# Kernel tuning notes

Hardware: AMD Instinct MI355X
Metric: run time of the kernel (lower is better)

## Reference

```python
import jax, jax.numpy as jnp
import numpy as np

N_OBJ, N_REL = 5000, 20000
HID, POOL, N_RELCLS, N_OBJCLS = 512, 4096, 51, 151


def setup_inputs() -> dict:
    key = jax.random.key(0)
    ks = jax.random.split(key, 8)
    s = lambda fi, fo: (2.0 / (fi + fo)) ** 0.5  # xavier-ish scale
    return {
        'edge_ctx': jax.random.normal(ks[0], (N_OBJ, HID), jnp.float32),
        'union_features': jax.random.normal(ks[1], (N_REL, POOL), jnp.float32),
        'W_pe': jax.random.normal(ks[2], (2 * HID, HID), jnp.float32) * (10.0 * (1.0 / HID) ** 0.5),
        'b_pe': jnp.zeros((2 * HID,), jnp.float32),
        'W_pc': jax.random.normal(ks[3], (POOL, 2 * HID), jnp.float32) * s(2 * HID, POOL),
        'b_pc': jnp.zeros((POOL,), jnp.float32),
        'W_cc': jax.random.normal(ks[4], (N_RELCLS, POOL), jnp.float32) * s(POOL, N_RELCLS),
        'b_cc': jnp.zeros((N_RELCLS,), jnp.float32),
        'freq_emb': jax.random.normal(ks[5], (N_OBJCLS * N_OBJCLS, N_RELCLS), jnp.float32) * 0.1,
        'obj_preds': jax.random.randint(ks[6], (N_OBJ,), 0, N_OBJCLS, jnp.int64 if jax.config.jax_enable_x64 else jnp.int32),
        'pair_idx': jax.random.randint(ks[7], (N_REL, 2), 0, N_OBJ, jnp.int64 if jax.config.jax_enable_x64 else jnp.int32),
    }


def reference(edge_ctx, union_features, W_pe, b_pe, W_pc, b_pc, W_cc, b_cc,
              freq_emb, obj_preds, pair_idx):
    # post_emb -> relu -> split into head/tail halves ([N,2,HID] view)
    edge_rep = jax.nn.relu(edge_ctx @ W_pe.T + b_pe)          # [N, 2*HID]
    head_rep, tail_rep = edge_rep[:, :HID], edge_rep[:, HID:]

    hi, ti = pair_idx[:, 0], pair_idx[:, 1]
    prod = jnp.concatenate([head_rep[hi], tail_rep[ti]], axis=-1)  # [R, 2*HID]
    prod_rep = prod @ W_pc.T + b_pc                               # [R, POOL]

    ctx_dists = (prod_rep * union_features) @ W_cc.T + b_cc      # [R, 51]

    # frequency bias: embedding lookup at head_cls * num_obj_cls + tail_cls
    pair_lbl = obj_preds[hi] * N_OBJCLS + obj_preds[ti]
    frq_dists = freq_emb[pair_lbl]                               # [R, 51]
    # dropout p=0.3 is identity in eval mode
    return ctx_dists + frq_dists
```

## Files before the change

### kernel.cpp

```cpp
#include <hip/hip_runtime.h>

typedef unsigned short u16;
typedef unsigned int u32;
typedef __attribute__((ext_vector_type(4))) float f32x4;
typedef __attribute__((ext_vector_type(8))) __bf16 bf16x8;
typedef __attribute__((ext_vector_type(8))) u16 u16x8;

__device__ __forceinline__ u16 f2bf(float x) {
  u32 u = __float_as_uint(x);
  u32 r = (u + 0x7FFFu + ((u >> 16) & 1u)) >> 16;
  return (u16)r;
}

__device__ __forceinline__ float bf2f(u16 b) {
  return __uint_as_float((u32)b << 16);
}

__device__ __forceinline__ void gl16(const void* g, void* l) {
  auto* gp = (__attribute__((address_space(1))) u32*)(g);
  auto* lp = (__attribute__((address_space(3))) u32*)(l);
  __builtin_amdgcn_global_load_lds(gp, lp, 16, 0, 0);
}

__device__ __forceinline__ f32x4 mfma16(bf16x8 a, bf16x8 b, f32x4 c) {
  return __builtin_amdgcn_mfma_f32_16x16x32_bf16(a, b, c, 0, 0, 0);
}

__device__ __forceinline__ u16x8 cvt8(const float* p) {
  float4 a = *(const float4*)p, b = *(const float4*)(p + 4);
  u16x8 v;
  v[0] = f2bf(a.x); v[1] = f2bf(a.y); v[2] = f2bf(a.z); v[3] = f2bf(a.w);
  v[4] = f2bf(b.x); v[5] = f2bf(b.y); v[6] = f2bf(b.z); v[7] = f2bf(b.w);
  return v;
}

__global__ void k_prep(const float* __restrict__ ec, const float* __restrict__ wpe,
                       const float* __restrict__ wpc, const float* __restrict__ wcc,
                       u16* __restrict__ ecb, u16* __restrict__ wpeb,
                       u16* __restrict__ wpcb, u16* __restrict__ wccb) {
  int i = blockIdx.x * 256 + threadIdx.x;
  if (i < 320000) {
    *(u16x8*)(ecb + (long)i * 8) = cvt8(ec + (long)i * 8);
  } else if (i < 385536) {
    int j = i - 320000;
    *(u16x8*)(wpeb + (long)j * 8) = cvt8(wpe + (long)j * 8);
  } else if (i < 909824) {
    int j = i - 385536;
    *(u16x8*)(wpcb + (long)j * 8) = cvt8(wpc + (long)j * 8);
  } else if (i < 942592) {
    int j = i - 909824;
    long base = (long)j * 8;
    int row = (int)(base >> 12);
    int col = (int)(base & 4095);
    u16x8 v;
    if (row < 51) {
      v = cvt8(wcc + (long)row * 4096 + col);
    } else {
#pragma unroll
      for (int k = 0; k < 8; ++k) v[k] = 0;
    }
    *(u16x8*)(wccb + base) = v;
  }
}

__device__ __forceinline__ void cstep(const char* sA, const char* sB,
                                      const int (&aOff)[4], const int (&bOff)[4],
                                      f32x4 (&acc)[4][4]) {
  bf16x8 af[4], bv[4];
#pragma unroll
  for (int mi = 0; mi < 4; ++mi) af[mi] = *(const bf16x8*)(sA + aOff[mi]);
#pragma unroll
  for (int ni = 0; ni < 4; ++ni) bv[ni] = *(const bf16x8*)(sB + bOff[ni]);
  __builtin_amdgcn_s_setprio(1);
#pragma unroll
  for (int mi = 0; mi < 4; ++mi)
#pragma unroll
    for (int ni = 0; ni < 4; ++ni)
      acc[mi][ni] = mfma16(af[mi], bv[ni], acc[mi][ni]);
  __builtin_amdgcn_s_setprio(0);
}

__device__ __forceinline__ void cstep64(const char* buf,
                                        const int (&aOff)[4][2], const int (&bOff)[4][2],
                                        f32x4 (&acc)[4][4]) {
  bf16x8 af[4][2], bv[4][2];
#pragma unroll
  for (int mi = 0; mi < 4; ++mi)
#pragma unroll
    for (int ks = 0; ks < 2; ++ks) af[mi][ks] = *(const bf16x8*)(buf + aOff[mi][ks]);
#pragma unroll
  for (int ni = 0; ni < 4; ++ni)
#pragma unroll
    for (int ks = 0; ks < 2; ++ks) bv[ni][ks] = *(const bf16x8*)(buf + bOff[ni][ks]);
  __builtin_amdgcn_s_setprio(1);
#pragma unroll
  for (int ks = 0; ks < 2; ++ks)
#pragma unroll
    for (int mi = 0; mi < 4; ++mi)
#pragma unroll
      for (int ni = 0; ni < 4; ++ni)
        acc[mi][ni] = mfma16(af[mi][ks], bv[ni][ks], acc[mi][ni]);
  __builtin_amdgcn_s_setprio(0);
}

__global__ __launch_bounds__(256, 2) void k_gemm1(const u16* __restrict__ A, const u16* __restrict__ B,
                                                  const float* __restrict__ bias, u16* __restrict__ outp) {
  __shared__ char lds[65536];
  int bx = blockIdx.x;
  int rb = bx >> 3, nb = bx & 7;
  int rowBase = rb * 128, nBase = nb * 128;
  int t = threadIdx.x, lane = t & 63, wid = t >> 6;
  int wr = wid >> 1, wc = wid & 1, lm = lane & 15, lg = lane >> 4;
  int ar0 = t >> 2, ar1 = 64 + ar0, c4 = t & 3;
  int sw0 = (c4 * 16) ^ (((ar0 >> 1) & 3) << 4);
  int sw1 = (c4 * 16) ^ (((ar1 >> 1) & 3) << 4);
  const char* aS0 = (const char*)(A + (long)min(rowBase + ar0, 4999) * 512) + sw0;
  const char* aS1 = (const char*)(A + (long)min(rowBase + ar1, 4999) * 512) + sw1;
  const char* bS0 = (const char*)(B + (long)(nBase + ar0) * 512) + sw0;
  const char* bS1 = (const char*)(B + (long)(nBase + ar1) * 512) + sw1;
  int t16 = t * 16;
  int aOff[4], bOff[4];
#pragma unroll
  for (int mi = 0; mi < 4; ++mi) { int r = wr * 64 + mi * 16 + lm; aOff[mi] = r * 64 + ((lg * 16) ^ (((r >> 1) & 3) << 4)); }
#pragma unroll
  for (int ni = 0; ni < 4; ++ni) { int r = wc * 64 + ni * 16 + lm; bOff[ni] = r * 64 + ((lg * 16) ^ (((r >> 1) & 3) << 4)); }
  f32x4 acc[4][4] = {};

#define STAGE_G(k, sb) do { \
    gl16(aS0 + (k) * 2, (sb) + t16); gl16(aS1 + (k) * 2, (sb) + 4096 + t16); \
    gl16(bS0 + (k) * 2, (sb) + 8192 + t16); gl16(bS1 + (k) * 2, (sb) + 12288 + t16); \
  } while (0)

  STAGE_G(0, lds);
  STAGE_G(32, lds + 16384);
  STAGE_G(64, lds + 32768);

  int cur = 0, stg = 3;
  for (int kt = 0; kt < 16; ++kt) {
    if (kt < 13) {
      char* sb = lds + stg * 16384;
      STAGE_G((kt + 3) * 32, sb);
    }
    if (kt < 13)       asm volatile("s_waitcnt vmcnt(12)" ::: "memory");
    else if (kt == 13) asm volatile("s_waitcnt vmcnt(8)" ::: "memory");
    else if (kt == 14) asm volatile("s_waitcnt vmcnt(4)" ::: "memory");
    else               asm volatile("s_waitcnt vmcnt(0)" ::: "memory");
    __builtin_amdgcn_s_barrier();
    char* cb = lds + cur * 16384;
    cstep(cb, cb + 8192, aOff, bOff, acc);
    __builtin_amdgcn_s_barrier();
    cur = (cur == 3) ? 0 : cur + 1;
    stg = (stg == 3) ? 0 : stg + 1;
  }
#undef STAGE_G

#pragma unroll
  for (int mi = 0; mi < 4; ++mi)
#pragma unroll
    for (int ni = 0; ni < 4; ++ni) {
      int n = nBase + wc * 64 + ni * 16 + lm;
      float bvv = bias[n];
#pragma unroll
      for (int rg = 0; rg < 4; ++rg) {
        int r = rowBase + wr * 64 + mi * 16 + lg * 4 + rg;
        if (r < 5000) {
          float v = acc[mi][ni][rg] + bvv;
          v = v > 0.f ? v : 0.f;
          outp[(long)r * 1024 + n] = f2bf(v);
        }
      }
    }
}

__global__ __launch_bounds__(256, 2) void k_gemm2(const u16* __restrict__ erep, const u16* __restrict__ wpc,
                                                  const float* __restrict__ bpc, u16* __restrict__ Hout,
                                                  u16* __restrict__ Tout) {
  __shared__ char lds[65536];
  int bx = blockIdx.x;
  int h = (bx >= 1280) ? 1 : 0;
  int rr = bx - h * 1280;
  int rb = rr >> 5, nb = rr & 31;
  int rowBase = rb * 128, nBase = nb * 128;
  u16* outp = h ? Tout : Hout;
  int t = threadIdx.x, lane = t & 63, wid = t >> 6;
  int wr = wid >> 1, wc = wid & 1, lm = lane & 15, lg = lane >> 4;
  int ar = t >> 3, c8 = t & 7;
  int srcswz = ((c8 ^ (ar & 7)) << 4);
  const char* aP[4];
  const char* bP[4];
#pragma unroll
  for (int i = 0; i < 4; ++i) {
    int Ra = min(rowBase + i * 32 + ar, 4999);
    aP[i] = (const char*)(erep + (long)Ra * 1024 + h * 512) + srcswz;
    int Rb = nBase + i * 32 + ar;
    bP[i] = (const char*)(wpc + (long)Rb * 1024 + h * 512) + srcswz;
  }
  int t16 = t * 16;
  int aOff[4][2], bOff[4][2];
#pragma unroll
  for (int mi = 0; mi < 4; ++mi)
#pragma unroll
    for (int ks = 0; ks < 2; ++ks) {
      int r = wr * 64 + mi * 16 + lm;
      aOff[mi][ks] = r * 128 + (((ks * 4 + lg) ^ (r & 7)) << 4);
    }
#pragma unroll
  for (int ni = 0; ni < 4; ++ni)
#pragma unroll
    for (int ks = 0; ks < 2; ++ks) {
      int r = wc * 64 + ni * 16 + lm;
      bOff[ni][ks] = 16384 + r * 128 + (((ks * 4 + lg) ^ (r & 7)) << 4);
    }
  f32x4 acc[4][4] = {};

#define STAGE2(kk, buf) do { \
    _Pragma("unroll") \
    for (int i = 0; i < 4; ++i) { \
      gl16(aP[i] + (kk) * 2, (buf) + i * 4096 + t16); \
      gl16(bP[i] + (kk) * 2, (buf) + 16384 + i * 4096 + t16); \
    } \
  } while (0)

  STAGE2(0, lds);
  for (int kt = 0; kt < 8; ++kt) {
    if (kt < 7) STAGE2((kt + 1) * 64, lds + (((kt + 1) & 1) ? 32768 : 0));
    if (kt < 7) asm volatile("s_waitcnt vmcnt(8)" ::: "memory");
    else        asm volatile("s_waitcnt vmcnt(0)" ::: "memory");
    __builtin_amdgcn_s_barrier();
    cstep64(lds + ((kt & 1) ? 32768 : 0), aOff, bOff, acc);
    __builtin_amdgcn_s_barrier();
  }
#undef STAGE2

#pragma unroll
  for (int mi = 0; mi < 4; ++mi)
#pragma unroll
    for (int ni = 0; ni < 4; ++ni) {
      int n = nBase + wc * 64 + ni * 16 + lm;
      float bvv = h ? 0.f : bpc[n];
#pragma unroll
      for (int rg = 0; rg < 4; ++rg) {
        int r = rowBase + wr * 64 + mi * 16 + lg * 4 + rg;
        if (r < 5000) {
          float v = acc[mi][ni][rg] + bvv;
          outp[(long)r * 4096 + n] = f2bf(v);
        }
      }
    }
}

__global__ __launch_bounds__(256) void k_final(
    const u16* __restrict__ H, const u16* __restrict__ T,
    const u16* __restrict__ wcc,
    const float* __restrict__ un,
    const int* __restrict__ pidx,
    float* __restrict__ partial) {
  __shared__ char sU[2][16384];
  int bx = blockIdx.x;
  int rb = bx >> 3, ps = bx & 7;
  int rowBase = rb * 64;
  int t = threadIdx.x, lane = t & 63, wid = t >> 6;
  int lm = lane & 15, lg = lane >> 4;
  int r16 = t >> 4, c16 = t & 15;

  u32 hoff[4], toff[4], uoff[4];
#pragma unroll
  for (int p = 0; p < 4; ++p) {
    int rG = min(rowBase + p * 16 + r16, 19999);
    hoff[p] = (u32)pidx[2 * rG] * 8192u + (u32)c16 * 16u;
    toff[p] = (u32)pidx[2 * rG + 1] * 8192u + (u32)c16 * 16u;
    uoff[p] = (u32)rG * 16384u + (u32)c16 * 32u;
  }
  const char* Hc = (const char*)H;
  const char* Tc = (const char*)T;
  const char* Uc = (const char*)un;
  int pc0 = ps * 512;

  u16x8 h8[4], t8[4];
  float4 u0[4], u1[4];

#define ISSUE(pcB) do { \
    _Pragma("unroll") \
    for (int p = 0; p < 4; ++p) { \
      h8[p] = *(const u16x8*)(Hc + hoff[p] + (u32)(pcB) * 2u); \
      t8[p] = *(const u16x8*)(Tc + toff[p] + (u32)(pcB) * 2u); \
      u0[p] = *(const float4*)(Uc + uoff[p] + (u32)(pcB) * 4u); \
      u1[p] = *(const float4*)(Uc + uoff[p] + (u32)(pcB) * 4u + 16u); \
    } \
  } while (0)

  f32x4 outAcc[4] = {};

  ISSUE(pc0);

  for (int chk = 0; chk < 4; ++chk) {
    int pcBase = pc0 + chk * 128;
    asm volatile("s_waitcnt vmcnt(0)" ::: "memory");
    char* sUb = sU[chk & 1];
#pragma unroll
    for (int p = 0; p < 4; ++p) {
      int r = p * 16 + r16;
      float uu[8];
      *(float4*)(uu) = u0[p];
      *(float4*)(uu + 4) = u1[p];
      bf16x8 pv;
#pragma unroll
      for (int j = 0; j < 8; ++j)
        pv[j] = (__bf16)((bf2f(h8[p][j]) + bf2f(t8[p][j])) * uu[j]);
      *(bf16x8*)(sUb + r * 256 + ((c16 * 16) ^ ((r & 7) << 4))) = pv;
    }
    bf16x8 bW[4][4];
#pragma unroll
    for (int kb = 0; kb < 4; ++kb)
#pragma unroll
      for (int ni = 0; ni < 4; ++ni)
        bW[kb][ni] = *(const bf16x8*)(wcc + (long)(ni * 16 + lm) * 4096 + pcBase + kb * 32 + lg * 8);
    if (chk < 3) ISSUE(pcBase + 128);
    asm volatile("s_waitcnt lgkmcnt(0)" ::: "memory");
    __builtin_amdgcn_s_barrier();

#pragma unroll
    for (int kb = 0; kb < 4; ++kb) {
      int r = wid * 16 + lm;
      bf16x8 aU = *(const bf16x8*)(sUb + r * 256 + ((kb * 64 + lg * 16) ^ ((r & 7) << 4)));
      __builtin_amdgcn_s_setprio(1);
#pragma unroll
      for (int ni = 0; ni < 4; ++ni)
        outAcc[ni] = mfma16(aU, bW[kb][ni], outAcc[ni]);
      __builtin_amdgcn_s_setprio(0);
    }
  }
#undef ISSUE

#pragma unroll
  for (int rg = 0; rg < 4; ++rg) {
    int r = wid * 16 + lg * 4 + rg;
    int rG = rowBase + r;
    if (rG < 20000) {
      long base = ((long)ps * 20000 + rG) * 64;
#pragma unroll
      for (int ni = 0; ni < 4; ++ni) {
        int c = ni * 16 + lm;
        if (c < 51) partial[base + c] = outAcc[ni][rg];
      }
    }
  }
}

__global__ void k_red(const float* __restrict__ partial, const float* __restrict__ bcc,
                      const float* __restrict__ freq, const int* __restrict__ preds,
                      const int* __restrict__ pidx, float* __restrict__ outp) {
  int idx = blockIdx.x * 256 + threadIdx.x;
  if (idx >= 20000 * 64) return;
  int row = idx >> 6, c = idx & 63;
  if (c >= 51) return;
  float s = 0.f;
#pragma unroll
  for (int i = 0; i < 8; ++i) s += partial[((long)i * 20000 + row) * 64 + c];
  int lbl = preds[pidx[2 * row]] * 151 + preds[pidx[2 * row + 1]];
  outp[(long)row * 51 + c] = s + bcc[c] + freq[(long)lbl * 51 + c];
}

extern "C" void kernel_launch(void* const* d_in, const int* in_sizes, int n_in,
                              void* d_out, int out_size, void* d_ws, size_t ws_size,
                              hipStream_t stream) {
  const float* edge_ctx = (const float*)d_in[0];
  const float* unionf   = (const float*)d_in[1];
  const float* W_pe     = (const float*)d_in[2];
  const float* b_pe     = (const float*)d_in[3];
  const float* W_pc     = (const float*)d_in[4];
  const float* b_pc     = (const float*)d_in[5];
  const float* W_cc     = (const float*)d_in[6];
  const float* b_cc     = (const float*)d_in[7];
  const float* freq     = (const float*)d_in[8];
  const int*   preds    = (const int*)d_in[9];
  const int*   pidx     = (const int*)d_in[10];
  float* out = (float*)d_out;
  char* ws = (char*)d_ws;

  u16* Hb    = (u16*)(ws + 0);
  u16* Tb    = (u16*)(ws + 40960000);
  u16* erep  = (u16*)(ws + 81920000);
  u16* wpcb  = (u16*)(ws + 92160000);
  u16* wccb  = (u16*)(ws + 100548608);
  u16* ecb   = (u16*)(ws + 101072896);
  u16* wpeb  = (u16*)(ws + 106192896);
  float* par = (float*)(ws + 107241472);

  k_prep<<<3682, 256, 0, stream>>>(edge_ctx, W_pe, W_pc, W_cc, ecb, wpeb, wpcb, wccb);
  k_gemm1<<<320, 256, 0, stream>>>(ecb, wpeb, b_pe, erep);
  k_gemm2<<<2560, 256, 0, stream>>>(erep, wpcb, b_pc, Hb, Tb);
  k_final<<<2504, 256, 0, stream>>>(Hb, Tb, wccb, unionf, pidx, par);
  k_red<<<5000, 256, 0, stream>>>(par, b_cc, freq, preds, pidx, out);
}
```

Baseline: 260.4 us.

## Switch gemm2 to 4-stage K=32 LDS pipeline reusing gemm1 step

```diff
diff --git a/kernel.cpp b/kernel.cpp
--- a/kernel.cpp
+++ b/kernel.cpp
@@ -80,29 +80,6 @@
   __builtin_amdgcn_s_setprio(0);
 }
 
-__device__ __forceinline__ void cstep64(const char* buf,
-                                        const int (&aOff)[4][2], const int (&bOff)[4][2],
-                                        f32x4 (&acc)[4][4]) {
-  bf16x8 af[4][2], bv[4][2];
-#pragma unroll
-  for (int mi = 0; mi < 4; ++mi)
-#pragma unroll
-    for (int ks = 0; ks < 2; ++ks) af[mi][ks] = *(const bf16x8*)(buf + aOff[mi][ks]);
-#pragma unroll
-  for (int ni = 0; ni < 4; ++ni)
-#pragma unroll
-    for (int ks = 0; ks < 2; ++ks) bv[ni][ks] = *(const bf16x8*)(buf + bOff[ni][ks]);
-  __builtin_amdgcn_s_setprio(1);
-#pragma unroll
-  for (int ks = 0; ks < 2; ++ks)
-#pragma unroll
-    for (int mi = 0; mi < 4; ++mi)
-#pragma unroll
-      for (int ni = 0; ni < 4; ++ni)
-        acc[mi][ni] = mfma16(af[mi][ks], bv[ni][ks], acc[mi][ni]);
-  __builtin_amdgcn_s_setprio(0);
-}
-
 __global__ __launch_bounds__(256, 2) void k_gemm1(const u16* __restrict__ A, const u16* __restrict__ B,
                                                   const float* __restrict__ bias, u16* __restrict__ outp) {
   __shared__ char lds[65536];
@@ -184,53 +161,48 @@
   u16* outp = h ? Tout : Hout;
   int t = threadIdx.x, lane = t & 63, wid = t >> 6;
   int wr = wid >> 1, wc = wid & 1, lm = lane & 15, lg = lane >> 4;
-  int ar = t >> 3, c8 = t & 7;
-  int srcswz = ((c8 ^ (ar & 7)) << 4);
-  const char* aP[4];
-  const char* bP[4];
-#pragma unroll
-  for (int i = 0; i < 4; ++i) {
-    int Ra = min(rowBase + i * 32 + ar, 4999);
-    aP[i] = (const char*)(erep + (long)Ra * 1024 + h * 512) + srcswz;
-    int Rb = nBase + i * 32 + ar;
-    bP[i] = (const char*)(wpc + (long)Rb * 1024 + h * 512) + srcswz;
-  }
+  int ar0 = t >> 2, ar1 = 64 + ar0, c4 = t & 3;
+  int sw0 = (c4 * 16) ^ (((ar0 >> 1) & 3) << 4);
+  int sw1 = (c4 * 16) ^ (((ar1 >> 1) & 3) << 4);
+  const char* aS0 = (const char*)(erep + (long)min(rowBase + ar0, 4999) * 1024 + h * 512) + sw0;
+  const char* aS1 = (const char*)(erep + (long)min(rowBase + ar1, 4999) * 1024 + h * 512) + sw1;
+  const char* bS0 = (const char*)(wpc + (long)(nBase + ar0) * 1024 + h * 512) + sw0;
+  const char* bS1 = (const char*)(wpc + (long)(nBase + ar1) * 1024 + h * 512) + sw1;
   int t16 = t * 16;
-  int aOff[4][2], bOff[4][2];
-#pragma unroll
-  for (int mi = 0; mi < 4; ++mi)
-#pragma unroll
-    for (int ks = 0; ks < 2; ++ks) {
-      int r = wr * 64 + mi * 16 + lm;
-      aOff[mi][ks] = r * 128 + (((ks * 4 + lg) ^ (r & 7)) << 4);
-    }
-#pragma unroll
-  for (int ni = 0; ni < 4; ++ni)
-#pragma unroll
-    for (int ks = 0; ks < 2; ++ks) {
-      int r = wc * 64 + ni * 16 + lm;
-      bOff[ni][ks] = 16384 + r * 128 + (((ks * 4 + lg) ^ (r & 7)) << 4);
-    }
+  int aOff[4], bOff[4];
+#pragma unroll
+  for (int mi = 0; mi < 4; ++mi) { int r = wr * 64 + mi * 16 + lm; aOff[mi] = r * 64 + ((lg * 16) ^ (((r >> 1) & 3) << 4)); }
+#pragma unroll
+  for (int ni = 0; ni < 4; ++ni) { int r = wc * 64 + ni * 16 + lm; bOff[ni] = r * 64 + ((lg * 16) ^ (((r >> 1) & 3) << 4)); }
   f32x4 acc[4][4] = {};
 
-#define STAGE2(kk, buf) do { \
-    _Pragma("unroll") \
-    for (int i = 0; i < 4; ++i) { \
-      gl16(aP[i] + (kk) * 2, (buf) + i * 4096 + t16); \
-      gl16(bP[i] + (kk) * 2, (buf) + 16384 + i * 4096 + t16); \
-    } \
+#define STAGE_G2(k, sb) do { \
+    gl16(aS0 + (k) * 2, (sb) + t16); gl16(aS1 + (k) * 2, (sb) + 4096 + t16); \
+    gl16(bS0 + (k) * 2, (sb) + 8192 + t16); gl16(bS1 + (k) * 2, (sb) + 12288 + t16); \
   } while (0)
 
-  STAGE2(0, lds);
-  for (int kt = 0; kt < 8; ++kt) {
-    if (kt < 7) STAGE2((kt + 1) * 64, lds + (((kt + 1) & 1) ? 32768 : 0));
-    if (kt < 7) asm volatile("s_waitcnt vmcnt(8)" ::: "memory");
-    else        asm volatile("s_waitcnt vmcnt(0)" ::: "memory");
-    __builtin_amdgcn_s_barrier();
-    cstep64(lds + ((kt & 1) ? 32768 : 0), aOff, bOff, acc);
-    __builtin_amdgcn_s_barrier();
-  }
-#undef STAGE2
+  STAGE_G2(0, lds);
+  STAGE_G2(32, lds + 16384);
+  STAGE_G2(64, lds + 32768);
+
+  int cur = 0, stg = 3;
+  for (int kt = 0; kt < 16; ++kt) {
+    if (kt < 13) {
+      char* sb = lds + stg * 16384;
+      STAGE_G2((kt + 3) * 32, sb);
+    }
+    if (kt < 13)       asm volatile("s_waitcnt vmcnt(12)" ::: "memory");
+    else if (kt == 13) asm volatile("s_waitcnt vmcnt(8)" ::: "memory");
+    else if (kt == 14) asm volatile("s_waitcnt vmcnt(4)" ::: "memory");
+    else               asm volatile("s_waitcnt vmcnt(0)" ::: "memory");
+    __builtin_amdgcn_s_barrier();
+    char* cb = lds + cur * 16384;
+    cstep(cb, cb + 8192, aOff, bOff, acc);
+    __builtin_amdgcn_s_barrier();
+    cur = (cur == 3) ? 0 : cur + 1;
+    stg = (stg == 3) ? 0 : stg + 1;
+  }
+#undef STAGE_G2
 
 #pragma unroll
   for (int mi = 0; mi < 4; ++mi)
```

New measurement: 263.4 us. No clear change (+1.1%).
